# Kernel tuning notes

Hardware: AMD Instinct MI355X
Metric: run time of the kernel (lower is better)

Reference implementation:

```python
import jax, jax.numpy as jnp
import numpy as np

N = 4096
F_IN = 512
ALPHA = 0.2          # LeakyReLU negative slope
NEG_INF = -9e15      # mask fill used by pyGAT


def setup_inputs() -> dict:
    key = jax.random.key(0)
    ks = jax.random.split(key, 9)
    x = jax.random.normal(ks[0], (N, F_IN), dtype=jnp.float32)
    adj = (jax.random.uniform(ks[1], (N, N)) < 0.005).astype(jnp.float32)
    adj = jnp.maximum(adj, jnp.eye(N, dtype=jnp.float32))
    s = 0.05
    W1 = jax.random.normal(ks[2], (512, 8, 128), dtype=jnp.float32) * s
    a_src1 = jax.random.normal(ks[3], (8, 128), dtype=jnp.float32) * s
    a_dst1 = jax.random.normal(ks[4], (8, 128), dtype=jnp.float32) * s
    W2 = jax.random.normal(ks[5], (1024, 1, 16), dtype=jnp.float32) * s
    a_src2 = jax.random.normal(ks[6], (1, 16), dtype=jnp.float32) * s
    a_dst2 = jax.random.normal(ks[7], (1, 16), dtype=jnp.float32) * s
    return {"x": x, "adj": adj, "W1": W1, "a_src1": a_src1, "a_dst1": a_dst1,
            "W2": W2, "a_src2": a_src2, "a_dst2": a_dst2}


def gat_layer(x, mask, W, a_src, a_dst, concat, activation):
    # x: [N, Fin], W: [Fin, H, Fout]
    h = jnp.einsum('nf,fho->nho', x, W)                  # [N, H, Fout]
    f_src = jnp.einsum('nho,ho->hn', h, a_src)            # [H, N]
    f_dst = jnp.einsum('nho,ho->hn', h, a_dst)            # [H, N]
    e = f_src[:, :, None] + f_dst[:, None, :]             # [H, N, N]
    e = jax.nn.leaky_relu(e, ALPHA)
    e = jnp.where(mask[None, :, :], e, NEG_INF)
    attn = jax.nn.softmax(e, axis=-1)                     # masked softmax over neighbors j
    out = jnp.einsum('hij,jho->iho', attn, h)             # [N, H, Fout]
    if concat:
        out = out.reshape(out.shape[0], -1)               # [N, H*Fout]
    else:
        out = out.mean(axis=1)                            # [N, Fout]
    if activation:
        out = jax.nn.elu(out)
    return out


def reference(x, adj, W1, a_src1, a_dst1, W2, a_src2, a_dst2):
    mask = adj > 0
    h1 = gat_layer(x, mask, W1, a_src1, a_dst1, concat=True, activation=True)
    h2 = gat_layer(h1, mask, W2, a_src2, a_dst2, concat=False, activation=False)
    out = jax.nn.elu(h2)
    return jax.nn.log_softmax(out, axis=1)
```

## Files before the change

### kernel.cpp

```cpp
#include <hip/hip_runtime.h>
#include <hip/hip_bf16.h>
#include <hip/hip_fp16.h>

typedef __attribute__((ext_vector_type(8))) short short8;
typedef __attribute__((ext_vector_type(8))) _Float16 half8;
typedef __attribute__((ext_vector_type(4))) float f32x4;

#define MAXNBR 128
#define ALPHA 0.2f

static __device__ __forceinline__ unsigned short f2h(float f) {
    return __half_as_ushort(__float2half(f));
}
static __device__ __forceinline__ float h2f(unsigned short u) {
    return __half2float(__ushort_as_half(u));
}

__global__ __launch_bounds__(256) void cvt(const float* __restrict__ x,
                                           unsigned short* __restrict__ xh,
                                           const float* __restrict__ W1,
                                           unsigned short* __restrict__ W1t) {
    int b = blockIdx.x, t = threadIdx.x;
    if (b < 1024) {
        size_t base = (size_t)b * 2048 + t * 8;
        float4 v0 = *(const float4*)&x[base];
        float4 v1 = *(const float4*)&x[base + 4];
        short8 o;
        o[0] = f2h(v0.x); o[1] = f2h(v0.y); o[2] = f2h(v0.z); o[3] = f2h(v0.w);
        o[4] = f2h(v1.x); o[5] = f2h(v1.y); o[6] = f2h(v1.z); o[7] = f2h(v1.w);
        *(short8*)&xh[base] = o;
    } else {
        int idx = (b - 1024) * 256 + t;
        int c = idx >> 9, k = idx & 511;
        W1t[idx] = f2h(W1[(size_t)k * 1024 + c]);
    }
}

__global__ __launch_bounds__(256) void gemm_scan(const unsigned short* __restrict__ A,
                                                 const unsigned short* __restrict__ Bt,
                                                 unsigned short* __restrict__ C,
                                                 const float* __restrict__ adj,
                                                 int* __restrict__ nbr_idx,
                                                 int* __restrict__ nbr_cnt) {
    __shared__ unsigned short Asm[128 * 64];
    __shared__ unsigned short Bsm[64 * 64];
    int b = blockIdx.x;
    int tid = threadIdx.x;
    if (b < 512) {
        int lane = tid & 63;
        int w = tid >> 6;
        int wr = w >> 1, wc = w & 1;
        int rowBase = (b & 31) * 128, colBase = (b >> 5) * 64;
        int lr = lane >> 3;
        int lc = (lane & 7) * 8;
        f32x4 acc[4][2] = {};
        for (int k0 = 0; k0 < 512; k0 += 64) {
            #pragma unroll
            for (int i = 0; i < 4; ++i) {
                int rA = i * 32 + w * 8;
                __builtin_amdgcn_global_load_lds(
                    (const __attribute__((address_space(1))) void*)&A[(size_t)(rowBase + rA + lr) * 512 + k0 + lc],
                    (__attribute__((address_space(3))) void*)&Asm[rA * 64],
                    16, 0, 0);
            }
            #pragma unroll
            for (int i = 0; i < 2; ++i) {
                int rB = i * 32 + w * 8;
                __builtin_amdgcn_global_load_lds(
                    (const __attribute__((address_space(1))) void*)&Bt[(size_t)(colBase + rB + lr) * 512 + k0 + lc],
                    (__attribute__((address_space(3))) void*)&Bsm[rB * 64],
                    16, 0, 0);
            }
            __syncthreads();
            #pragma unroll
            for (int kk = 0; kk < 64; kk += 32) {
                half8 af[4], bfv[2];
                int kf = kk + (lane >> 4) * 8;
                #pragma unroll
                for (int m = 0; m < 4; ++m)
                    af[m] = *(const half8*)&Asm[(wr * 64 + m * 16 + (lane & 15)) * 64 + kf];
                #pragma unroll
                for (int n = 0; n < 2; ++n)
                    bfv[n] = *(const half8*)&Bsm[(wc * 32 + n * 16 + (lane & 15)) * 64 + kf];
                #pragma unroll
                for (int m = 0; m < 4; ++m)
                    #pragma unroll
                    for (int n = 0; n < 2; ++n)
                        acc[m][n] = __builtin_amdgcn_mfma_f32_16x16x32_f16(af[m], bfv[n], acc[m][n], 0, 0, 0);
            }
            __syncthreads();
        }
        int crow0 = rowBase + wr * 64, ccol0 = colBase + wc * 32;
        #pragma unroll
        for (int m = 0; m < 4; ++m)
            #pragma unroll
            for (int n = 0; n < 2; ++n) {
                int col = ccol0 + n * 16 + (lane & 15);
                int row0 = crow0 + m * 16 + (lane >> 4) * 4;
                #pragma unroll
                for (int r = 0; r < 4; ++r)
                    C[(size_t)(row0 + r) * 1024 + col] = f2h(acc[m][n][r]);
            }
    } else {
        int row = (b - 512) * 4 + (tid >> 6);
        int lane = tid & 63;
        const float* arow = adj + (size_t)row * 4096;
        int cnt = 0;
        for (int base = 0; base < 4096; base += 256) {
            float4 v = *(const float4*)&arow[base + lane * 4];
            #pragma unroll
            for (int s = 0; s < 4; ++s) {
                float xv = ((const float*)&v)[s];
                unsigned long long m = __ballot(xv > 0.f);
                if (xv > 0.f) {
                    int pos = cnt + (int)__popcll(m & ((1ull << lane) - 1ull));
                    if (pos < MAXNBR) nbr_idx[row * MAXNBR + pos] = base + lane * 4 + s;
                }
                cnt += (int)__popcll(m);
            }
        }
        if (lane == 0) nbr_cnt[row] = cnt < MAXNBR ? cnt : MAXNBR;
    }
}

__global__ __launch_bounds__(256) void attn_coef1(const unsigned short* __restrict__ h1h,
                                                  const float* __restrict__ a_src,
                                                  const float* __restrict__ a_dst,
                                                  float* __restrict__ f_src,
                                                  float* __restrict__ f_dst) {
    int n = blockIdx.x, t = threadIdx.x;
    ushort4 v = *(const ushort4*)&h1h[(size_t)n * 1024 + t * 4];
    int head = t >> 5;
    int o0 = (t * 4) & 127;
    float hv0 = h2f(v.x), hv1 = h2f(v.y), hv2 = h2f(v.z), hv3 = h2f(v.w);
    float ps = hv0 * a_src[head * 128 + o0] + hv1 * a_src[head * 128 + o0 + 1]
             + hv2 * a_src[head * 128 + o0 + 2] + hv3 * a_src[head * 128 + o0 + 3];
    float pd = hv0 * a_dst[head * 128 + o0] + hv1 * a_dst[head * 128 + o0 + 1]
             + hv2 * a_dst[head * 128 + o0 + 2] + hv3 * a_dst[head * 128 + o0 + 3];
    #pragma unroll
    for (int off = 1; off < 32; off <<= 1) {
        ps += __shfl_xor(ps, off);
        pd += __shfl_xor(pd, off);
    }
    if ((t & 31) == 0) {
        f_src[head * 4096 + n] = ps;
        f_dst[head * 4096 + n] = pd;
    }
}

__global__ __launch_bounds__(256, 8) void aggregate4(const unsigned short* __restrict__ h1h,
                                                     const int* __restrict__ nbr_idx,
                                                     const int* __restrict__ nbr_cnt,
                                                     const float* __restrict__ f_src,
                                                     const float* __restrict__ f_dst,
                                                     unsigned short* __restrict__ h1act) {
    __shared__ int nbr[MAXNBR];
    __shared__ float attw[8][MAXNBR];
    __shared__ float part[2][64][8];
    int i = blockIdx.x;
    int t = threadIdx.x;
    int lane = t & 63;
    int w = t >> 6;
    int cnt = nbr_cnt[i];
    if (t < MAXNBR) nbr[t] = (t < cnt) ? nbr_idx[i * MAXNBR + t] : 0;
    __syncthreads();
    {
        int h = t >> 5, sl = t & 31;
        float fsh = f_src[h * 4096 + i];
        float e[4];
        #pragma unroll
        for (int p = 0; p < 4; ++p) {
            int j = sl + p * 32;
            if (j < cnt) {
                float xv = fsh + f_dst[h * 4096 + nbr[j]];
                e[p] = xv > 0.f ? xv : ALPHA * xv;
            } else e[p] = -INFINITY;
        }
        float m = fmaxf(fmaxf(e[0], e[1]), fmaxf(e[2], e[3]));
        #pragma unroll
        for (int off = 1; off < 32; off <<= 1) m = fmaxf(m, __shfl_xor(m, off));
        float wq[4], s = 0.f;
        #pragma unroll
        for (int p = 0; p < 4; ++p) {
            wq[p] = (e[p] == -INFINITY) ? 0.f : __expf(e[p] - m);
            s += wq[p];
        }
        #pragma unroll
        for (int off = 1; off < 32; off <<= 1) s += __shfl_xor(s, off);
        float inv = 1.f / s;
        #pragma unroll
        for (int p = 0; p < 4; ++p) attw[h][sl + p * 32] = wq[p] * inv;
    }
    __syncthreads();
    int par = w & 1, half = w >> 1;
    int head = half * 4 + (lane >> 4);
    const unsigned short* src = h1h + half * 512 + lane * 8;
    float acc[8] = {0.f, 0.f, 0.f, 0.f, 0.f, 0.f, 0.f, 0.f};
    int cntPad = (cnt + 3) & ~3;
    for (int j = par; j < cntPad; j += 4) {
        int nb1 = nbr[j], nb2 = nbr[j + 2];
        float w1 = attw[head][j], w2 = attw[head][j + 2];
        half8 v1 = *(const half8*)&src[(size_t)nb1 << 10];
        half8 v2 = *(const half8*)&src[(size_t)nb2 << 10];
        #pragma unroll
        for (int k = 0; k < 8; ++k)
            acc[k] += w1 * (float)v1[k] + w2 * (float)v2[k];
    }
    if (par == 1) {
        #pragma unroll
        for (int k = 0; k < 8; ++k) part[half][lane][k] = acc[k];
    }
    __syncthreads();
    if (par == 0) {
        short8 o;
        #pragma unroll
        for (int k = 0; k < 8; ++k) {
            float a = acc[k] + part[half][lane][k];
            a = a > 0.f ? a : (__expf(a) - 1.f);
            o[k] = f2h(a);
        }
        *(short8*)&h1act[(size_t)i * 1024 + half * 512 + lane * 8] = o;
    }
}

__global__ __launch_bounds__(256) void layer2_mfma(const unsigned short* __restrict__ h1act,
                                                   const float* __restrict__ W2,
                                                   const float* __restrict__ a_src2,
                                                   const float* __restrict__ a_dst2,
                                                   float* __restrict__ h2,
                                                   float* __restrict__ f_src2,
                                                   float* __restrict__ f_dst2) {
    __shared__ unsigned short Asm2[64 * 64];
    __shared__ unsigned short W2t[16 * 1032];
    int t = threadIdx.x, lane = t & 63, w = t >> 6;
    int rowBase = blockIdx.x * 64;
    for (int idx = t; idx < 16384; idx += 256) {
        int k = idx >> 4, o = idx & 15;
        W2t[o * 1032 + k] = f2h(W2[idx]);
    }
    f32x4 acc = {};
    __syncthreads();
    for (int k0 = 0; k0 < 1024; k0 += 64) {
        #pragma unroll
        for (int r = 0; r < 2; ++r) {
            int rA = r * 32 + w * 8;
            __builtin_amdgcn_global_load_lds(
                (const __attribute__((address_space(1))) void*)&h1act[(size_t)(rowBase + rA + (lane >> 3)) * 1024 + k0 + (lane & 7) * 8],
                (__attribute__((address_space(3))) void*)&Asm2[rA * 64],
                16, 0, 0);
        }
        __syncthreads();
        #pragma unroll
        for (int kk = 0; kk < 64; kk += 32) {
            half8 af = *(const half8*)&Asm2[(w * 16 + (lane & 15)) * 64 + kk + (lane >> 4) * 8];
            half8 bf = *(const half8*)&W2t[(lane & 15) * 1032 + k0 + kk + (lane >> 4) * 8];
            acc = __builtin_amdgcn_mfma_f32_16x16x32_f16(af, bf, acc, 0, 0, 0);
        }
        __syncthreads();
    }
    int col = lane & 15;
    int g = lane >> 4;
    #pragma unroll
    for (int r = 0; r < 4; ++r) {
        int row = rowBase + w * 16 + g * 4 + r;
        float v = acc[r];
        h2[row * 16 + col] = v;
        float ps = v * a_src2[col];
        float pd = v * a_dst2[col];
        #pragma unroll
        for (int off = 1; off < 16; off <<= 1) {
            ps += __shfl_xor(ps, off);
            pd += __shfl_xor(pd, off);
        }
        if (col == 0) { f_src2[row] = ps; f_dst2[row] = pd; }
    }
}

__global__ __launch_bounds__(64) void final_layer(const float* __restrict__ h2,
                                                  const int* __restrict__ nbr_idx,
                                                  const int* __restrict__ nbr_cnt,
                                                  const float* __restrict__ f_src2,
                                                  const float* __restrict__ f_dst2,
                                                  float* __restrict__ out) {
    __shared__ float attn[MAXNBR];
    __shared__ int nbr[MAXNBR];
    int i = blockIdx.x;
    int l = threadIdx.x;
    int cnt = nbr_cnt[i];
    float fsi = f_src2[i];
    for (int j = l; j < MAXNBR; j += 64) {
        float e = -INFINITY;
        if (j < cnt) {
            int jj = nbr_idx[i * MAXNBR + j];
            nbr[j] = jj;
            float xv = fsi + f_dst2[jj];
            e = xv > 0.f ? xv : ALPHA * xv;
        }
        attn[j] = e;
    }
    __syncthreads();
    float m = fmaxf(attn[l], attn[l + 64]);
    #pragma unroll
    for (int off = 1; off < 64; off <<= 1) m = fmaxf(m, __shfl_xor(m, off));
    float s = 0.f;
    {
        float e0 = attn[l], e1 = attn[l + 64];
        if (e0 != -INFINITY) s += __expf(e0 - m);
        if (e1 != -INFINITY) s += __expf(e1 - m);
    }
    #pragma unroll
    for (int off = 1; off < 64; off <<= 1) s += __shfl_xor(s, off);
    for (int j = l; j < MAXNBR; j += 64) {
        float e = attn[j];
        attn[j] = (e == -INFINITY) ? 0.f : __expf(e - m) / s;
    }
    __syncthreads();
    if (l < 16) {
        float acc = 0.f;
        for (int j = 0; j < cnt; ++j)
            acc += attn[j] * h2[nbr[j] * 16 + l];
        float v = acc > 0.f ? acc : expm1f(acc);
        float mx = v;
        #pragma unroll
        for (int off = 1; off < 16; off <<= 1) mx = fmaxf(mx, __shfl_xor(mx, off));
        float se = __expf(v - mx);
        #pragma unroll
        for (int off = 1; off < 16; off <<= 1) se += __shfl_xor(se, off);
        out[i * 16 + l] = v - mx - logf(se);
    }
}

extern "C" void kernel_launch(void* const* d_in, const int* in_sizes, int n_in,
                              void* d_out, int out_size, void* d_ws, size_t ws_size,
                              hipStream_t stream) {
    const float* x      = (const float*)d_in[0];
    const float* adj    = (const float*)d_in[1];
    const float* W1     = (const float*)d_in[2];
    const float* a_src1 = (const float*)d_in[3];
    const float* a_dst1 = (const float*)d_in[4];
    const float* W2     = (const float*)d_in[5];
    const float* a_src2 = (const float*)d_in[6];
    const float* a_dst2 = (const float*)d_in[7];
    float* out = (float*)d_out;

    char* ws = (char*)d_ws;
    unsigned short* xh    = (unsigned short*)ws;
    unsigned short* w1t   = (unsigned short*)(ws + (4u << 20));
    unsigned short* h1h   = (unsigned short*)(ws + (6u << 20));
    unsigned short* h1act = (unsigned short*)(ws + (26u << 20));
    float* fsrc1 = (float*)(ws + (14u << 20));
    float* fdst1 = (float*)(ws + (14u << 20) + (128u << 10));
    float* h2    = (float*)(ws + (15u << 20));
    float* fsrc2 = (float*)(ws + (15u << 20) + (256u << 10));
    float* fdst2 = (float*)(ws + (15u << 20) + (272u << 10));
    int* nbr_idx = (int*)(ws + (16u << 20));
    int* nbr_cnt = (int*)(ws + (18u << 20));

    cvt<<<3072, 256, 0, stream>>>(x, xh, W1, w1t);
    gemm_scan<<<1536, 256, 0, stream>>>(xh, w1t, h1h, adj, nbr_idx, nbr_cnt);
    attn_coef1<<<4096, 256, 0, stream>>>(h1h, a_src1, a_dst1, fsrc1, fdst1);
    aggregate4<<<4096, 256, 0, stream>>>(h1h, nbr_idx, nbr_cnt, fsrc1, fdst1, h1act);
    layer2_mfma<<<64, 256, 0, stream>>>(h1act, W2, a_src2, a_dst2, h2, fsrc2, fdst2);
    final_layer<<<4096, 64, 0, stream>>>(h2, nbr_idx, nbr_cnt, fsrc2, fdst2, out);
}
```

Measured before the change: 74.62 us.

## Use node-major attention coefficients and fp16 packed accumulation in aggregation

Attention source/destination coefficients are stored node-major ([N][8]) so each neighbor's eight head values are fetched with two float4 loads, and the edge scores are computed once into shared memory. The aggregation loop now keeps fp16 attention weights and accumulates with packed half2 FMAs instead of converting to fp32. Layer-2 coefficients are packed as float2 to halve the gathers in the final layer. Accumulating in fp16 reduces ALU and conversion work but risks precision loss.

```diff
diff --git a/kernel.cpp b/kernel.cpp
--- a/kernel.cpp
+++ b/kernel.cpp
@@ -4,6 +4,7 @@
 
 typedef __attribute__((ext_vector_type(8))) short short8;
 typedef __attribute__((ext_vector_type(8))) _Float16 half8;
+typedef __attribute__((ext_vector_type(2))) _Float16 h2v;
 typedef __attribute__((ext_vector_type(4))) float f32x4;
 
 #define MAXNBR 128
@@ -126,8 +127,8 @@
 __global__ __launch_bounds__(256) void attn_coef1(const unsigned short* __restrict__ h1h,
                                                   const float* __restrict__ a_src,
                                                   const float* __restrict__ a_dst,
-                                                  float* __restrict__ f_src,
-                                                  float* __restrict__ f_dst) {
+                                                  float* __restrict__ fsp,
+                                                  float* __restrict__ fdp) {
     int n = blockIdx.x, t = threadIdx.x;
     ushort4 v = *(const ushort4*)&h1h[(size_t)n * 1024 + t * 4];
     int head = t >> 5;
@@ -143,39 +144,54 @@
         pd += __shfl_xor(pd, off);
     }
     if ((t & 31) == 0) {
-        f_src[head * 4096 + n] = ps;
-        f_dst[head * 4096 + n] = pd;
-    }
-}
-
-__global__ __launch_bounds__(256, 8) void aggregate4(const unsigned short* __restrict__ h1h,
+        fsp[n * 8 + head] = ps;
+        fdp[n * 8 + head] = pd;
+    }
+}
+
+__global__ __launch_bounds__(256, 8) void aggregate5(const unsigned short* __restrict__ h1h,
                                                      const int* __restrict__ nbr_idx,
                                                      const int* __restrict__ nbr_cnt,
-                                                     const float* __restrict__ f_src,
-                                                     const float* __restrict__ f_dst,
+                                                     const float* __restrict__ fsp,
+                                                     const float* __restrict__ fdp,
                                                      unsigned short* __restrict__ h1act) {
     __shared__ int nbr[MAXNBR];
-    __shared__ float attw[8][MAXNBR];
-    __shared__ float part[2][64][8];
+    __shared__ float e_s[8][MAXNBR];
+    __shared__ _Float16 attwS[8][MAXNBR];
+    __shared__ half8 partS[128];
     int i = blockIdx.x;
     int t = threadIdx.x;
-    int lane = t & 63;
-    int w = t >> 6;
     int cnt = nbr_cnt[i];
     if (t < MAXNBR) nbr[t] = (t < cnt) ? nbr_idx[i * MAXNBR + t] : 0;
     __syncthreads();
+    if (t < MAXNBR) {
+        if (t < cnt) {
+            int nb = nbr[t];
+            float4 fs0 = *(const float4*)&fsp[i * 8];
+            float4 fs1 = *(const float4*)&fsp[i * 8 + 4];
+            float4 d0 = *(const float4*)&fdp[nb * 8];
+            float4 d1 = *(const float4*)&fdp[nb * 8 + 4];
+            float e0 = fs0.x + d0.x, e1 = fs0.y + d0.y, e2 = fs0.z + d0.z, e3 = fs0.w + d0.w;
+            float e4 = fs1.x + d1.x, e5 = fs1.y + d1.y, e6 = fs1.z + d1.z, e7 = fs1.w + d1.w;
+            e_s[0][t] = e0 > 0.f ? e0 : ALPHA * e0;
+            e_s[1][t] = e1 > 0.f ? e1 : ALPHA * e1;
+            e_s[2][t] = e2 > 0.f ? e2 : ALPHA * e2;
+            e_s[3][t] = e3 > 0.f ? e3 : ALPHA * e3;
+            e_s[4][t] = e4 > 0.f ? e4 : ALPHA * e4;
+            e_s[5][t] = e5 > 0.f ? e5 : ALPHA * e5;
+            e_s[6][t] = e6 > 0.f ? e6 : ALPHA * e6;
+            e_s[7][t] = e7 > 0.f ? e7 : ALPHA * e7;
+        } else {
+            #pragma unroll
+            for (int h = 0; h < 8; ++h) e_s[h][t] = -INFINITY;
+        }
+    }
+    __syncthreads();
     {
         int h = t >> 5, sl = t & 31;
-        float fsh = f_src[h * 4096 + i];
         float e[4];
         #pragma unroll
-        for (int p = 0; p < 4; ++p) {
-            int j = sl + p * 32;
-            if (j < cnt) {
-                float xv = fsh + f_dst[h * 4096 + nbr[j]];
-                e[p] = xv > 0.f ? xv : ALPHA * xv;
-            } else e[p] = -INFINITY;
-        }
+        for (int p = 0; p < 4; ++p) e[p] = e_s[h][sl + p * 32];
         float m = fmaxf(fmaxf(e[0], e[1]), fmaxf(e[2], e[3]));
         #pragma unroll
         for (int off = 1; off < 32; off <<= 1) m = fmaxf(m, __shfl_xor(m, off));
@@ -189,37 +205,48 @@
         for (int off = 1; off < 32; off <<= 1) s += __shfl_xor(s, off);
         float inv = 1.f / s;
         #pragma unroll
-        for (int p = 0; p < 4; ++p) attw[h][sl + p * 32] = wq[p] * inv;
-    }
-    __syncthreads();
-    int par = w & 1, half = w >> 1;
-    int head = half * 4 + (lane >> 4);
-    const unsigned short* src = h1h + half * 512 + lane * 8;
-    float acc[8] = {0.f, 0.f, 0.f, 0.f, 0.f, 0.f, 0.f, 0.f};
+        for (int p = 0; p < 4; ++p)
+            attwS[h][sl + p * 32] = (_Float16)(wq[p] * inv);
+    }
+    __syncthreads();
+    int tf = t & 127;
+    int par = t >> 7;
+    int head = tf >> 4;
+    const unsigned short* src = h1h + tf * 8;
+    h2v acc2[4] = {};
     int cntPad = (cnt + 3) & ~3;
     for (int j = par; j < cntPad; j += 4) {
         int nb1 = nbr[j], nb2 = nbr[j + 2];
-        float w1 = attw[head][j], w2 = attw[head][j + 2];
+        _Float16 w1 = attwS[head][j], w2 = attwS[head][j + 2];
         half8 v1 = *(const half8*)&src[(size_t)nb1 << 10];
         half8 v2 = *(const half8*)&src[(size_t)nb2 << 10];
-        #pragma unroll
-        for (int k = 0; k < 8; ++k)
-            acc[k] += w1 * (float)v1[k] + w2 * (float)v2[k];
+        h2v w1v = (h2v){w1, w1}, w2v = (h2v){w2, w2};
+        const h2v* p1 = (const h2v*)&v1;
+        const h2v* p2 = (const h2v*)&v2;
+        #pragma unroll
+        for (int q = 0; q < 4; ++q)
+            acc2[q] += w1v * p1[q] + w2v * p2[q];
     }
     if (par == 1) {
-        #pragma unroll
-        for (int k = 0; k < 8; ++k) part[half][lane][k] = acc[k];
+        half8 st;
+        #pragma unroll
+        for (int q = 0; q < 4; ++q) { st[q * 2] = acc2[q][0]; st[q * 2 + 1] = acc2[q][1]; }
+        partS[tf] = st;
     }
     __syncthreads();
     if (par == 0) {
+        half8 p = partS[tf];
         short8 o;
         #pragma unroll
-        for (int k = 0; k < 8; ++k) {
-            float a = acc[k] + part[half][lane][k];
-            a = a > 0.f ? a : (__expf(a) - 1.f);
-            o[k] = f2h(a);
-        }
-        *(short8*)&h1act[(size_t)i * 1024 + half * 512 + lane * 8] = o;
+        for (int q = 0; q < 4; ++q) {
+            float a0 = (float)acc2[q][0] + (float)p[q * 2];
+            float a1 = (float)acc2[q][1] + (float)p[q * 2 + 1];
+            a0 = a0 > 0.f ? a0 : (__expf(a0) - 1.f);
+            a1 = a1 > 0.f ? a1 : (__expf(a1) - 1.f);
+            o[q * 2] = f2h(a0);
+            o[q * 2 + 1] = f2h(a1);
+        }
+        *(short8*)&h1act[(size_t)i * 1024 + tf * 8] = o;
     }
 }
 
@@ -228,8 +255,7 @@
                                                    const float* __restrict__ a_src2,
                                                    const float* __restrict__ a_dst2,
                                                    float* __restrict__ h2,
-                                                   float* __restrict__ f_src2,
-                                                   float* __restrict__ f_dst2) {
+                                                   float2* __restrict__ fsd2) {
     __shared__ unsigned short Asm2[64 * 64];
     __shared__ unsigned short W2t[16 * 1032];
     int t = threadIdx.x, lane = t & 63, w = t >> 6;
@@ -272,28 +298,27 @@
             ps += __shfl_xor(ps, off);
             pd += __shfl_xor(pd, off);
         }
-        if (col == 0) { f_src2[row] = ps; f_dst2[row] = pd; }
+        if (col == 0) fsd2[row] = make_float2(ps, pd);
     }
 }
 
 __global__ __launch_bounds__(64) void final_layer(const float* __restrict__ h2,
                                                   const int* __restrict__ nbr_idx,
                                                   const int* __restrict__ nbr_cnt,
-                                                  const float* __restrict__ f_src2,
-                                                  const float* __restrict__ f_dst2,
+                                                  const float2* __restrict__ fsd2,
                                                   float* __restrict__ out) {
     __shared__ float attn[MAXNBR];
     __shared__ int nbr[MAXNBR];
     int i = blockIdx.x;
     int l = threadIdx.x;
     int cnt = nbr_cnt[i];
-    float fsi = f_src2[i];
+    float fsi = fsd2[i].x;
     for (int j = l; j < MAXNBR; j += 64) {
         float e = -INFINITY;
         if (j < cnt) {
             int jj = nbr_idx[i * MAXNBR + j];
             nbr[j] = jj;
-            float xv = fsi + f_dst2[jj];
+            float xv = fsi + fsd2[jj].y;
             e = xv > 0.f ? xv : ALPHA * xv;
         }
         attn[j] = e;
@@ -347,19 +372,18 @@
     unsigned short* xh    = (unsigned short*)ws;
     unsigned short* w1t   = (unsigned short*)(ws + (4u << 20));
     unsigned short* h1h   = (unsigned short*)(ws + (6u << 20));
-    unsigned short* h1act = (unsigned short*)(ws + (26u << 20));
-    float* fsrc1 = (float*)(ws + (14u << 20));
-    float* fdst1 = (float*)(ws + (14u << 20) + (128u << 10));
+    float* fsp   = (float*)(ws + (14u << 20));
+    float* fdp   = (float*)(ws + (14u << 20) + (128u << 10));
     float* h2    = (float*)(ws + (15u << 20));
-    float* fsrc2 = (float*)(ws + (15u << 20) + (256u << 10));
-    float* fdst2 = (float*)(ws + (15u << 20) + (272u << 10));
+    float2* fsd2 = (float2*)(ws + (15u << 20) + (256u << 10));
     int* nbr_idx = (int*)(ws + (16u << 20));
     int* nbr_cnt = (int*)(ws + (18u << 20));
+    unsigned short* h1act = (unsigned short*)(ws + (26u << 20));
 
     cvt<<<3072, 256, 0, stream>>>(x, xh, W1, w1t);
     gemm_scan<<<1536, 256, 0, stream>>>(xh, w1t, h1h, adj, nbr_idx, nbr_cnt);
-    attn_coef1<<<4096, 256, 0, stream>>>(h1h, a_src1, a_dst1, fsrc1, fdst1);
-    aggregate4<<<4096, 256, 0, stream>>>(h1h, nbr_idx, nbr_cnt, fsrc1, fdst1, h1act);
-    layer2_mfma<<<64, 256, 0, stream>>>(h1act, W2, a_src2, a_dst2, h2, fsrc2, fdst2);
-    final_layer<<<4096, 64, 0, stream>>>(h2, nbr_idx, nbr_cnt, fsrc2, fdst2, out);
-}
+    attn_coef1<<<4096, 256, 0, stream>>>(h1h, a_src1, a_dst1, fsp, fdp);
+    aggregate5<<<4096, 256, 0, stream>>>(h1h, nbr_idx, nbr_cnt, fsp, fdp, h1act);
+    layer2_mfma<<<64, 256, 0, stream>>>(h1act, W2, a_src2, a_dst2, h2, fsd2);
+    final_layer<<<4096, 64, 0, stream>>>(h2, nbr_idx, nbr_cnt, fsd2, out);
+}
```

Measured after the change: 72.95 us. 1.02x faster.
